# Kernel optimization log

Hardware: AMD Instinct MI355X
Metric: run time of the kernel (lower is better)

Reference implementation:

```python
import jax, jax.numpy as jnp
import numpy as np

# Config constants (from CantorFusionConfigV2 defaults / init_kwargs)
NUM_HEADS = 8
HEAD_DIM = 64
K_NEIGHBORS = 64        # fusion_window
LEVELS = 5              # k_simplex + 1
TAU = 0.25
BASE = 3.0
ALPHA = 0.5
EPS = 1e-8
RESIDUAL_SCALE = 1.0


def _cantor_measure(S):
    """Vectorized Devil's Staircase Cantor measure for S positions in [0,1]. Returns [S]."""
    pos = (jnp.arange(S, dtype=jnp.float32) + 0.5) / S
    pos = jnp.clip(pos, 1e-10, 1.0 - 1e-10)
    ks = jnp.arange(1, LEVELS + 1, dtype=jnp.float32)
    scales = BASE ** ks                      # [L]
    lvl_w = 0.5 ** ks                        # [L]
    centers = jnp.array([0.5, 1.5, 2.5], dtype=jnp.float32)
    y = jnp.mod(pos[:, None] * scales, BASE)            # [S, L]
    logits = -((y[..., None] - centers) ** 2) / (TAU + 1e-10)  # [S, L, 3]
    p = jax.nn.softmax(logits, axis=-1)
    bits = p[..., 2] + ALPHA * p[..., 1]                # [S, L]
    return jnp.sum(bits * lvl_w, axis=-1)               # [S]


def _routes_and_weights(S):
    """KNN routes [S,K] by Cantor distance + inverse-distance softmax weights [S,K]."""
    cm = _cantor_measure(S)
    Dm = jnp.abs(cm[:, None] - cm[None, :])             # [S, S]
    Dm = Dm / (Dm.max() + 1e-10)
    neg_d, routes = jax.lax.top_k(-Dm, K_NEIGHBORS)     # k smallest distances
    route_dist = -neg_d                                  # [S, K]
    w = jax.nn.softmax(1.0 / (route_dist + EPS), axis=-1)
    return routes, w


def setup_inputs() -> dict:
    key = jax.random.key(0)
    k1, k2, k3 = jax.random.split(key, 3)
    B, S, D = 2, 2048, 512
    x = jax.random.normal(k1, (B, S, D), dtype=jnp.float32)
    W_in = jax.random.normal(k2, (D, D), dtype=jnp.float32) * (1.0 / np.sqrt(D))
    b_in = jnp.zeros((D,), dtype=jnp.float32)
    W_out = jax.random.normal(k3, (D, D), dtype=jnp.float32) * (1.0 / np.sqrt(D))
    b_out = jnp.zeros((D,), dtype=jnp.float32)
    return {"x": x, "W_in": W_in, "b_in": b_in, "W_out": W_out, "b_out": b_out}


def reference(x, W_in, b_in, W_out, b_out):
    B, S, dim = x.shape
    routes, w = _routes_and_weights(S)                   # [S,K], [S,K] (no-grad geometry)
    routes = jax.lax.stop_gradient(routes)
    w = jax.lax.stop_gradient(w)
    # input projection and head split -> [B, H, S, D]
    h = (x @ W_in + b_in).reshape(B, S, NUM_HEADS, HEAD_DIM).transpose(0, 2, 1, 3)
    # neighbor gather [B, H, S, K, D] then inverse-distance weighted sum
    gathered = h[:, :, routes, :]                        # [B,H,S,K,D]
    fused = jnp.einsum('bhskd,sk->bhsd', gathered, w)    # [B,H,S,D]
    out = fused.transpose(0, 2, 1, 3).reshape(B, S, dim) @ W_out + b_out
    return x + RESIDUAL_SCALE * out
```

## Files before the change

### kernel.cpp

```cpp
#include <hip/hip_runtime.h>
#include <hip/hip_bf16.h>

#define S_LEN 2048

typedef __attribute__((ext_vector_type(8))) short bf16x8;
typedef __attribute__((ext_vector_type(4))) float f32x4;
typedef __attribute__((ext_vector_type(4))) unsigned int u32x4;

__device__ inline unsigned short f2b(float f) {
    unsigned u = __builtin_bit_cast(unsigned, f);
    return (unsigned short)((u + 0x7FFFu + ((u >> 16) & 1u)) >> 16);
}

__device__ inline int swoff(int row, int k) {
    int o = row * 128 + k * 2;
    return o ^ ((row & 7) << 4);
}

__device__ inline float cantor_cm(int s) {
    float pos = ((float)s + 0.5f) * (1.0f / 2048.0f);
    float cm = 0.0f, scale = 1.0f, lvlw = 1.0f;
    #pragma unroll
    for (int k = 1; k <= 5; ++k) {
        scale *= 3.0f; lvlw *= 0.5f;
        float y = fmodf(pos * scale, 3.0f);
        float d0 = y - 0.5f, d1 = y - 1.5f, d2 = y - 2.5f;
        float l0 = -(d0 * d0) * 4.0f;
        float l1 = -(d1 * d1) * 4.0f;
        float l2 = -(d2 * d2) * 4.0f;
        float m = fmaxf(l0, fmaxf(l1, l2));
        float e0 = (float)exp((double)(l0 - m));
        float e1 = (float)exp((double)(l1 - m));
        float e2 = (float)exp((double)(l2 - m));
        float sum = (e0 + e1) + e2;
        float p1 = e1 / sum, p2 = e2 / sum;
        cm += (p2 + 0.5f * p1) * lvlw;
    }
    return cm;
}

__global__ __launch_bounds__(256) void prep2_kernel(
    const float* __restrict__ x,
    const float* __restrict__ W_in, const float* __restrict__ b_in,
    const float* __restrict__ W_out, const float* __restrict__ b_out,
    unsigned short* __restrict__ Wct, float* __restrict__ bc,
    unsigned short* __restrict__ xa) {
    __shared__ char lds[24576];
    const int b = blockIdx.x, tid = threadIdx.x;
    const int wid = tid >> 6, lane = tid & 63;
    const int l15 = lane & 15, l4 = lane >> 4;

    if (b < 64) {
        char* As = lds;
        char* Bs = lds + 8192;
        int bm = b >> 3, bn = b & 7;
        int wr = wid >> 1, wc = wid & 1;
        int an = tid & 63, ajg = tid >> 6;
        int bk = tid >> 2, bjq = (tid & 3) * 16;
        const float* acol = W_out + bm * 64 + an;
        const float* brow = W_in + (size_t)(bn * 64 + bk) * 512 + bjq;
        f32x4 acc[2][2] = {};
        for (int k0 = 0; k0 < 512; k0 += 64) {
            unsigned short ta[16];
            #pragma unroll
            for (int i = 0; i < 16; ++i)
                ta[i] = f2b(acol[(size_t)(k0 + ajg * 16 + i) * 512]);
            *(u32x4*)(As + swoff(an, ajg * 16))     = *(u32x4*)&ta[0];
            *(u32x4*)(As + swoff(an, ajg * 16 + 8)) = *(u32x4*)&ta[8];
            unsigned short tb[16];
            #pragma unroll
            for (int i = 0; i < 4; ++i) {
                float4 v = *(const float4*)(brow + k0 + i * 4);
                tb[i*4+0] = f2b(v.x); tb[i*4+1] = f2b(v.y);
                tb[i*4+2] = f2b(v.z); tb[i*4+3] = f2b(v.w);
            }
            *(u32x4*)(Bs + swoff(bk, bjq))     = *(u32x4*)&tb[0];
            *(u32x4*)(Bs + swoff(bk, bjq + 8)) = *(u32x4*)&tb[8];
            __syncthreads();
            #pragma unroll
            for (int kk = 0; kk < 2; ++kk) {
                const int kb = kk * 32 + l4 * 8;
                bf16x8 af[2], bg[2];
                #pragma unroll
                for (int m = 0; m < 2; ++m)
                    af[m] = *(bf16x8*)(As + swoff(wr * 32 + m * 16 + l15, kb));
                #pragma unroll
                for (int n = 0; n < 2; ++n)
                    bg[n] = *(bf16x8*)(Bs + swoff(wc * 32 + n * 16 + l15, kb));
                #pragma unroll
                for (int m = 0; m < 2; ++m)
                    #pragma unroll
                    for (int n = 0; n < 2; ++n)
                        acc[m][n] = __builtin_amdgcn_mfma_f32_16x16x32_bf16(
                            af[m], bg[n], acc[m][n], 0, 0, 0);
            }
            __syncthreads();
        }
        #pragma unroll
        for (int m = 0; m < 2; ++m)
            #pragma unroll
            for (int r = 0; r < 4; ++r) {
                int row = bm * 64 + wr * 32 + m * 16 + l4 * 4 + r;
                #pragma unroll
                for (int n = 0; n < 2; ++n) {
                    int col = bn * 64 + wc * 32 + n * 16 + l15;
                    Wct[(size_t)row * 512 + col] = f2b(acc[m][n][r]);
                }
            }
    } else if (b < 72) {
        float (*red)[64] = (float(*)[64])lds;
        int nl = tid & 63, jc = tid >> 6;
        int n = (b - 64) * 64 + nl;
        float acc = 0.0f;
        #pragma unroll 8
        for (int j = jc * 128; j < jc * 128 + 128; ++j)
            acc += b_in[j] * W_out[(size_t)j * 512 + n];
        red[jc][nl] = acc;
        __syncthreads();
        if (jc == 0)
            bc[n] = b_out[n] + ((red[0][nl] + red[1][nl]) +
                                (red[2][nl] + red[3][nl]));
    } else {
        float* cml = (float*)lds;
        int*   mem = (int*)(lds + 8192) + wid * 64;
        for (int i = tid; i < S_LEN; i += 256)
            cml[i] = cantor_cm(i);
        __syncthreads();
        int gbase = (b - 72) * 16 + wid * 4;
        for (int q = 0; q < 4; ++q) {
            int s = gbase + q;
            float v = cml[s];
            int n = 0;
            for (int j0 = 0; j0 < S_LEN; j0 += 64) {
                float c = cml[j0 + lane];
                bool m = (c == v);
                unsigned long long mask = __ballot(m);
                if (m) {
                    int idx = n + __popcll(mask & ((1ull << lane) - 1ull));
                    if (idx < 64) mem[idx] = j0 + lane;
                }
                n += __popcll(mask);
            }
            int gn = n < 64 ? n : 64;
            float a0[8] = {}, a1[8] = {};
            for (int e = 0; e < gn; ++e) {
                int r = mem[e];
                const float* p0 = x + (size_t)r * 512 + lane * 8;
                const float* p1 = p0 + (size_t)S_LEN * 512;
                float4 u0 = *(const float4*)p0, u1 = *(const float4*)(p0 + 4);
                float4 w0 = *(const float4*)p1, w1 = *(const float4*)(p1 + 4);
                a0[0] += u0.x; a0[1] += u0.y; a0[2] += u0.z; a0[3] += u0.w;
                a0[4] += u1.x; a0[5] += u1.y; a0[6] += u1.z; a0[7] += u1.w;
                a1[0] += w0.x; a1[1] += w0.y; a1[2] += w0.z; a1[3] += w0.w;
                a1[4] += w1.x; a1[5] += w1.y; a1[6] += w1.z; a1[7] += w1.w;
            }
            float gi = 1.0f / (float)gn;
            unsigned short t0[8], t1[8];
            #pragma unroll
            for (int i = 0; i < 8; ++i) {
                t0[i] = f2b(a0[i] * gi);
                t1[i] = f2b(a1[i] * gi);
            }
            *(u32x4*)(xa + (size_t)s * 512 + lane * 8)           = *(u32x4*)t0;
            *(u32x4*)(xa + (size_t)(S_LEN + s) * 512 + lane * 8) = *(u32x4*)t1;
        }
    }
}

__global__ __launch_bounds__(256) void gemmF_kernel(
    const float* __restrict__ x, const unsigned short* __restrict__ xa,
    const unsigned short* __restrict__ Wct, const float* __restrict__ bc,
    float* __restrict__ out) {
    __shared__ char lds[2 * 64 * 64 * 2];
    char* As = lds;
    char* Bs = lds + 64 * 64 * 2;
    const int tid = threadIdx.x;
    const int id = blockIdx.x;
    const int xcd = id & 7, slot = id >> 3;
    const int bm = xcd * 8 + (slot & 7);
    const int bn = slot >> 3;
    const int wid = tid >> 6, lane = tid & 63;
    const int wr = wid >> 1, wc = wid & 1;
    const int l15 = lane & 15, l4 = lane >> 4;
    const int arow = tid >> 2, akq = (tid & 3) * 16;

    const unsigned short* asrc = xa  + (size_t)(bm * 64 + arow) * 512 + akq;
    const unsigned short* bsrc = Wct + (size_t)(bn * 64 + arow) * 512 + akq;

    u32x4 arg[2], brg[2];
    auto la = [&](int k0) {
        arg[0] = *(const u32x4*)(asrc + k0);
        arg[1] = *(const u32x4*)(asrc + k0 + 8);
    };
    auto lb = [&](int k0) {
        brg[0] = *(const u32x4*)(bsrc + k0);
        brg[1] = *(const u32x4*)(bsrc + k0 + 8);
    };

    f32x4 acc[2][2] = {};
    la(0); lb(0);
    for (int k0 = 0; k0 < 512; k0 += 64) {
        *(u32x4*)(As + swoff(arow, akq))     = arg[0];
        *(u32x4*)(As + swoff(arow, akq + 8)) = arg[1];
        *(u32x4*)(Bs + swoff(arow, akq))     = brg[0];
        *(u32x4*)(Bs + swoff(arow, akq + 8)) = brg[1];
        __syncthreads();
        if (k0 + 64 < 512) { la(k0 + 64); lb(k0 + 64); }
        #pragma unroll
        for (int kk = 0; kk < 2; ++kk) {
            const int kb = kk * 32 + l4 * 8;
            bf16x8 af[2], bg[2];
            #pragma unroll
            for (int m = 0; m < 2; ++m)
                af[m] = *(bf16x8*)(As + swoff(wr * 32 + m * 16 + l15, kb));
            #pragma unroll
            for (int n = 0; n < 2; ++n)
                bg[n] = *(bf16x8*)(Bs + swoff(wc * 32 + n * 16 + l15, kb));
            #pragma unroll
            for (int m = 0; m < 2; ++m)
                #pragma unroll
                for (int n = 0; n < 2; ++n)
                    acc[m][n] = __builtin_amdgcn_mfma_f32_16x16x32_bf16(
                        af[m], bg[n], acc[m][n], 0, 0, 0);
        }
        __syncthreads();
    }

    float bv[2];
    #pragma unroll
    for (int n = 0; n < 2; ++n) bv[n] = bc[bn * 64 + wc * 32 + n * 16 + l15];
    #pragma unroll
    for (int m = 0; m < 2; ++m)
        #pragma unroll
        for (int r = 0; r < 4; ++r) {
            int row = bm * 64 + wr * 32 + m * 16 + l4 * 4 + r;
            #pragma unroll
            for (int n = 0; n < 2; ++n) {
                int col = bn * 64 + wc * 32 + n * 16 + l15;
                float v = acc[m][n][r] + bv[n];
                out[(size_t)row * 512 + col] = x[(size_t)row * 512 + col] + v;
            }
        }
}

extern "C" void kernel_launch(void* const* d_in, const int* in_sizes, int n_in,
                              void* d_out, int out_size, void* d_ws, size_t ws_size,
                              hipStream_t stream) {
    const float* x     = (const float*)d_in[0];
    const float* W_in  = (const float*)d_in[1];
    const float* b_in  = (const float*)d_in[2];
    const float* W_out = (const float*)d_in[3];
    const float* b_out = (const float*)d_in[4];
    float* out = (float*)d_out;

    char* ws = (char*)d_ws;
    unsigned short* Wct = (unsigned short*)ws;
    float*          bc  = (float*)(ws + 524288);
    unsigned short* xa  = (unsigned short*)(ws + 524288 + 4096);

    prep2_kernel<<<200, 256, 0, stream>>>(x, W_in, b_in, W_out, b_out,
                                          Wct, bc, xa);
    gemmF_kernel<<<512, 256, 0, stream>>>(x, xa, Wct, bc, out);
}
```

Baseline: 32.65 us.

## Double-buffer LDS in output GEMM with 128-wide K tiles

The output-projection GEMM kernel now stages 128-wide K tiles instead of 64-wide ones and uses two LDS buffers. This halves the number of K iterations and cuts one barrier per iteration, since the next tile is written to the other buffer after the MFMAs. LDS use grows to 64 KB per block, which can limit occupancy. Each thread also holds twice as many prefetch registers.

```diff
diff --git a/kernel.cpp b/kernel.cpp
--- a/kernel.cpp
+++ b/kernel.cpp
@@ -14,6 +14,10 @@
 
 __device__ inline int swoff(int row, int k) {
     int o = row * 128 + k * 2;
+    return o ^ ((row & 7) << 4);
+}
+__device__ inline int swoff2(int row, int k) {
+    int o = row * 256 + k * 2;
     return o ^ ((row & 7) << 4);
 }
 
@@ -171,9 +175,7 @@
     const float* __restrict__ x, const unsigned short* __restrict__ xa,
     const unsigned short* __restrict__ Wct, const float* __restrict__ bc,
     float* __restrict__ out) {
-    __shared__ char lds[2 * 64 * 64 * 2];
-    char* As = lds;
-    char* Bs = lds + 64 * 64 * 2;
+    __shared__ char lds[65536];
     const int tid = threadIdx.x;
     const int id = blockIdx.x;
     const int xcd = id & 7, slot = id >> 3;
@@ -182,40 +184,48 @@
     const int wid = tid >> 6, lane = tid & 63;
     const int wr = wid >> 1, wc = wid & 1;
     const int l15 = lane & 15, l4 = lane >> 4;
-    const int arow = tid >> 2, akq = (tid & 3) * 16;
-
-    const unsigned short* asrc = xa  + (size_t)(bm * 64 + arow) * 512 + akq;
-    const unsigned short* bsrc = Wct + (size_t)(bn * 64 + arow) * 512 + akq;
-
-    u32x4 arg[2], brg[2];
+    const int arow = tid >> 2, ak0 = (tid & 3) * 32;
+
+    const unsigned short* asrc = xa  + (size_t)(bm * 64 + arow) * 512 + ak0;
+    const unsigned short* bsrc = Wct + (size_t)(bn * 64 + arow) * 512 + ak0;
+
+    u32x4 arg[4], brg[4];
     auto la = [&](int k0) {
-        arg[0] = *(const u32x4*)(asrc + k0);
-        arg[1] = *(const u32x4*)(asrc + k0 + 8);
+        #pragma unroll
+        for (int i = 0; i < 4; ++i) arg[i] = *(const u32x4*)(asrc + k0 + i * 8);
     };
     auto lb = [&](int k0) {
-        brg[0] = *(const u32x4*)(bsrc + k0);
-        brg[1] = *(const u32x4*)(bsrc + k0 + 8);
+        #pragma unroll
+        for (int i = 0; i < 4; ++i) brg[i] = *(const u32x4*)(bsrc + k0 + i * 8);
+    };
+    auto st = [&](int buf) {
+        char* As = lds + buf * 32768;
+        char* Bs = As + 16384;
+        #pragma unroll
+        for (int i = 0; i < 4; ++i) {
+            *(u32x4*)(As + swoff2(arow, ak0 + i * 8)) = arg[i];
+            *(u32x4*)(Bs + swoff2(arow, ak0 + i * 8)) = brg[i];
+        }
     };
 
     f32x4 acc[2][2] = {};
     la(0); lb(0);
-    for (int k0 = 0; k0 < 512; k0 += 64) {
-        *(u32x4*)(As + swoff(arow, akq))     = arg[0];
-        *(u32x4*)(As + swoff(arow, akq + 8)) = arg[1];
-        *(u32x4*)(Bs + swoff(arow, akq))     = brg[0];
-        *(u32x4*)(Bs + swoff(arow, akq + 8)) = brg[1];
-        __syncthreads();
-        if (k0 + 64 < 512) { la(k0 + 64); lb(k0 + 64); }
-        #pragma unroll
-        for (int kk = 0; kk < 2; ++kk) {
+    st(0);
+    __syncthreads();
+    for (int t = 0; t < 4; ++t) {
+        if (t < 3) { la((t + 1) * 128); lb((t + 1) * 128); }
+        char* As = lds + (t & 1) * 32768;
+        char* Bs = As + 16384;
+        #pragma unroll
+        for (int kk = 0; kk < 4; ++kk) {
             const int kb = kk * 32 + l4 * 8;
             bf16x8 af[2], bg[2];
             #pragma unroll
             for (int m = 0; m < 2; ++m)
-                af[m] = *(bf16x8*)(As + swoff(wr * 32 + m * 16 + l15, kb));
+                af[m] = *(bf16x8*)(As + swoff2(wr * 32 + m * 16 + l15, kb));
             #pragma unroll
             for (int n = 0; n < 2; ++n)
-                bg[n] = *(bf16x8*)(Bs + swoff(wc * 32 + n * 16 + l15, kb));
+                bg[n] = *(bf16x8*)(Bs + swoff2(wc * 32 + n * 16 + l15, kb));
             #pragma unroll
             for (int m = 0; m < 2; ++m)
                 #pragma unroll
@@ -223,6 +233,7 @@
                     acc[m][n] = __builtin_amdgcn_mfma_f32_16x16x32_bf16(
                         af[m], bg[n], acc[m][n], 0, 0, 0);
         }
+        if (t < 3) st((t + 1) & 1);
         __syncthreads();
     }
 
```

Result: slower. 33.54 us (+2.7%).

## Precompute Cantor measure in separate kernel and halve GEMM M-tile to 32

Applied to the files above, without the earlier changes.

The Cantor measure computation, which uses double-precision exp and was previously repeated by all 128 gather blocks, moves into a tiny separate kernel whose output the gather blocks copy into LDS. The final GEMM uses a 32x64 tile instead of 64x64, doubling the grid to 1024 blocks, with launch bounds set for 4 blocks per CU to raise occupancy. The costs are an extra kernel launch and less data reuse per GEMM block.

```diff
diff --git a/kernel.cpp b/kernel.cpp
--- a/kernel.cpp
+++ b/kernel.cpp
@@ -17,7 +17,8 @@
     return o ^ ((row & 7) << 4);
 }
 
-__device__ inline float cantor_cm(int s) {
+__global__ __launch_bounds__(256) void cantor_kernel(float* __restrict__ cmf) {
+    int s = blockIdx.x * 256 + threadIdx.x;
     float pos = ((float)s + 0.5f) * (1.0f / 2048.0f);
     float cm = 0.0f, scale = 1.0f, lvlw = 1.0f;
     #pragma unroll
@@ -36,13 +37,14 @@
         float p1 = e1 / sum, p2 = e2 / sum;
         cm += (p2 + 0.5f * p1) * lvlw;
     }
-    return cm;
-}
-
-__global__ __launch_bounds__(256) void prep2_kernel(
+    cmf[s] = cm;
+}
+
+__global__ __launch_bounds__(256) void prep3_kernel(
     const float* __restrict__ x,
     const float* __restrict__ W_in, const float* __restrict__ b_in,
     const float* __restrict__ W_out, const float* __restrict__ b_out,
+    const float* __restrict__ cmf,
     unsigned short* __restrict__ Wct, float* __restrict__ bc,
     unsigned short* __restrict__ xa) {
     __shared__ char lds[24576];
@@ -123,8 +125,8 @@
     } else {
         float* cml = (float*)lds;
         int*   mem = (int*)(lds + 8192) + wid * 64;
-        for (int i = tid; i < S_LEN; i += 256)
-            cml[i] = cantor_cm(i);
+        for (int i = tid; i < 512; i += 256)
+            *(float4*)&cml[i * 4] = *(const float4*)&cmf[i * 4];
         __syncthreads();
         int gbase = (b - 72) * 16 + wid * 4;
         for (int q = 0; q < 4; ++q) {
@@ -167,61 +169,57 @@
     }
 }
 
-__global__ __launch_bounds__(256) void gemmF_kernel(
+__global__ __launch_bounds__(256, 4) void gemmF_kernel(
     const float* __restrict__ x, const unsigned short* __restrict__ xa,
     const unsigned short* __restrict__ Wct, const float* __restrict__ bc,
     float* __restrict__ out) {
-    __shared__ char lds[2 * 64 * 64 * 2];
+    __shared__ char lds[12288];
     char* As = lds;
-    char* Bs = lds + 64 * 64 * 2;
+    char* Bs = lds + 4096;
     const int tid = threadIdx.x;
     const int id = blockIdx.x;
     const int xcd = id & 7, slot = id >> 3;
-    const int bm = xcd * 8 + (slot & 7);
-    const int bn = slot >> 3;
+    const int bm = xcd * 16 + (slot & 15);
+    const int bn = slot >> 4;
     const int wid = tid >> 6, lane = tid & 63;
     const int wr = wid >> 1, wc = wid & 1;
     const int l15 = lane & 15, l4 = lane >> 4;
-    const int arow = tid >> 2, akq = (tid & 3) * 16;
-
-    const unsigned short* asrc = xa  + (size_t)(bm * 64 + arow) * 512 + akq;
-    const unsigned short* bsrc = Wct + (size_t)(bn * 64 + arow) * 512 + akq;
-
-    u32x4 arg[2], brg[2];
-    auto la = [&](int k0) {
-        arg[0] = *(const u32x4*)(asrc + k0);
-        arg[1] = *(const u32x4*)(asrc + k0 + 8);
-    };
+    const int arow = tid >> 3, akq = (tid & 7) * 8;
+    const int brow = tid >> 2, bkq = (tid & 3) * 16;
+
+    const unsigned short* asrc = xa  + (size_t)(bm * 32 + arow) * 512 + akq;
+    const unsigned short* bsrc = Wct + (size_t)(bn * 64 + brow) * 512 + bkq;
+
+    u32x4 arg, brg[2];
+    auto la = [&](int k0) { arg = *(const u32x4*)(asrc + k0); };
     auto lb = [&](int k0) {
         brg[0] = *(const u32x4*)(bsrc + k0);
         brg[1] = *(const u32x4*)(bsrc + k0 + 8);
     };
-
-    f32x4 acc[2][2] = {};
+    auto st = [&]() {
+        *(u32x4*)(As + swoff(arow, akq))     = arg;
+        *(u32x4*)(Bs + swoff(brow, bkq))     = brg[0];
+        *(u32x4*)(Bs + swoff(brow, bkq + 8)) = brg[1];
+    };
+
+    f32x4 acc[2] = {};
     la(0); lb(0);
-    for (int k0 = 0; k0 < 512; k0 += 64) {
-        *(u32x4*)(As + swoff(arow, akq))     = arg[0];
-        *(u32x4*)(As + swoff(arow, akq + 8)) = arg[1];
-        *(u32x4*)(Bs + swoff(arow, akq))     = brg[0];
-        *(u32x4*)(Bs + swoff(arow, akq + 8)) = brg[1];
-        __syncthreads();
-        if (k0 + 64 < 512) { la(k0 + 64); lb(k0 + 64); }
+    for (int t = 0; t < 8; ++t) {
+        st();
+        __syncthreads();
+        if (t < 7) { la((t + 1) * 64); lb((t + 1) * 64); }
         #pragma unroll
         for (int kk = 0; kk < 2; ++kk) {
             const int kb = kk * 32 + l4 * 8;
-            bf16x8 af[2], bg[2];
-            #pragma unroll
-            for (int m = 0; m < 2; ++m)
-                af[m] = *(bf16x8*)(As + swoff(wr * 32 + m * 16 + l15, kb));
+            bf16x8 af = *(bf16x8*)(As + swoff(wr * 16 + l15, kb));
+            bf16x8 bg[2];
             #pragma unroll
             for (int n = 0; n < 2; ++n)
                 bg[n] = *(bf16x8*)(Bs + swoff(wc * 32 + n * 16 + l15, kb));
             #pragma unroll
-            for (int m = 0; m < 2; ++m)
-                #pragma unroll
-                for (int n = 0; n < 2; ++n)
-                    acc[m][n] = __builtin_amdgcn_mfma_f32_16x16x32_bf16(
-                        af[m], bg[n], acc[m][n], 0, 0, 0);
+            for (int n = 0; n < 2; ++n)
+                acc[n] = __builtin_amdgcn_mfma_f32_16x16x32_bf16(
+                    af, bg[n], acc[n], 0, 0, 0);
         }
         __syncthreads();
     }
@@ -230,17 +228,15 @@
     #pragma unroll
     for (int n = 0; n < 2; ++n) bv[n] = bc[bn * 64 + wc * 32 + n * 16 + l15];
     #pragma unroll
-    for (int m = 0; m < 2; ++m)
+    for (int r = 0; r < 4; ++r) {
+        int row = bm * 32 + wr * 16 + l4 * 4 + r;
         #pragma unroll
-        for (int r = 0; r < 4; ++r) {
-            int row = bm * 64 + wr * 32 + m * 16 + l4 * 4 + r;
-            #pragma unroll
-            for (int n = 0; n < 2; ++n) {
-                int col = bn * 64 + wc * 32 + n * 16 + l15;
-                float v = acc[m][n][r] + bv[n];
-                out[(size_t)row * 512 + col] = x[(size_t)row * 512 + col] + v;
-            }
-        }
+        for (int n = 0; n < 2; ++n) {
+            int col = bn * 64 + wc * 32 + n * 16 + l15;
+            float v = acc[n][r] + bv[n];
+            out[(size_t)row * 512 + col] = x[(size_t)row * 512 + col] + v;
+        }
+    }
 }
 
 extern "C" void kernel_launch(void* const* d_in, const int* in_sizes, int n_in,
@@ -256,9 +252,11 @@
     char* ws = (char*)d_ws;
     unsigned short* Wct = (unsigned short*)ws;
     float*          bc  = (float*)(ws + 524288);
-    unsigned short* xa  = (unsigned short*)(ws + 524288 + 4096);
-
-    prep2_kernel<<<200, 256, 0, stream>>>(x, W_in, b_in, W_out, b_out,
-                                          Wct, bc, xa);
-    gemmF_kernel<<<512, 256, 0, stream>>>(x, xa, Wct, bc, out);
-}
+    float*          cmf = (float*)(ws + 524288 + 4096);
+    unsigned short* xa  = (unsigned short*)(ws + 524288 + 4096 + 8192);
+
+    cantor_kernel<<<8, 256, 0, stream>>>(cmf);
+    prep3_kernel<<<200, 256, 0, stream>>>(x, W_in, b_in, W_out, b_out,
+                                          cmf, Wct, bc, xa);
+    gemmF_kernel<<<1024, 256, 0, stream>>>(x, xa, Wct, bc, out);
+}
```

New measurement: 29.38 us, median of 3. 10.0% less time.
